# Optimization experiments

Hardware: AMD Instinct MI355X
Metric: run time of the kernel (lower is better)

Reference implementation:

```python
import jax, jax.numpy as jnp
import numpy as np

D_MODEL = 512
D_INNER = 1024           # expand=2 * d_model
HEADDIM = 1024           # headdim = 2*hidden_dim -> nheads = 1
NHEADS = 1
D_STATE = 128            # Mamba2 default
D_CONV = 4               # Mamba2 default
CONV_DIM = D_INNER + 2 * D_STATE   # 1280
D_IN_PROJ = 2 * D_INNER + 2 * D_STATE + NHEADS  # 2305
BATCH, SEQ = 8, 2048
EPS = 1e-5


def setup_inputs() -> dict:
    key = jax.random.key(0)
    ks = jax.random.split(key, 8)
    x = jax.random.normal(ks[0], (BATCH, SEQ, D_MODEL), dtype=jnp.float32)
    rnn_state = jnp.zeros((1, BATCH, D_MODEL), dtype=jnp.float32)
    W_in = jax.random.normal(ks[1], (D_MODEL, D_IN_PROJ), dtype=jnp.float32) * 0.02
    conv_w = jax.random.normal(ks[2], (CONV_DIM, D_CONV), dtype=jnp.float32) * 0.2
    conv_b = jnp.zeros((CONV_DIM,), dtype=jnp.float32)
    dt_bias = jax.random.normal(ks[3], (NHEADS,), dtype=jnp.float32) * 0.1
    # A in (-16, -1): A_log = log(uniform(1,16))
    A_log = jnp.log(jax.random.uniform(ks[4], (NHEADS,), minval=1.0, maxval=16.0, dtype=jnp.float32))
    D = jnp.ones((NHEADS,), dtype=jnp.float32)
    norm_w = jnp.ones((D_INNER,), dtype=jnp.float32)
    W_out = jax.random.normal(ks[5], (D_INNER, D_MODEL), dtype=jnp.float32) * 0.02
    return {"x": x, "rnn_state": rnn_state, "W_in": W_in, "conv_w": conv_w,
            "conv_b": conv_b, "dt_bias": dt_bias, "A_log": A_log, "D": D,
            "norm_w": norm_w, "W_out": W_out}


def _mamba2_forward(x, W_in, conv_w, conv_b, dt_bias, A_log, D, norm_w, W_out):
    Bsz, T, _ = x.shape
    zxbcdt = x @ W_in                              # [B,T,2305]
    z = zxbcdt[..., :D_INNER]                      # [B,T,1024]
    xBC = zxbcdt[..., D_INNER:D_INNER + CONV_DIM]  # [B,T,1280]
    dt = zxbcdt[..., -NHEADS:]                     # [B,T,1]

    # causal depthwise conv1d over time, then silu
    xBC_t = jnp.transpose(xBC, (0, 2, 1))          # [B,C,T]
    w = conv_w[:, None, :]                          # [C,1,K]
    conv = jax.lax.conv_general_dilated(
        xBC_t, w, window_strides=(1,), padding=[(D_CONV - 1, 0)],
        feature_group_count=CONV_DIM, dimension_numbers=("NCH", "OIH", "NCH"))
    xBC = jax.nn.silu(jnp.transpose(conv, (0, 2, 1)) + conv_b)  # [B,T,1280]

    x_ssm = xBC[..., :D_INNER].reshape(Bsz, T, NHEADS, HEADDIM)  # [B,T,H,P]
    Bm = xBC[..., D_INNER:D_INNER + D_STATE]       # [B,T,N] (ngroups=1)
    Cm = xBC[..., -D_STATE:]                       # [B,T,N]

    dt = jax.nn.softplus(dt + dt_bias)             # [B,T,H]
    A = -jnp.exp(A_log)                            # [H]

    # selective SSM recurrence over time (time-major scan)
    xs = (jnp.transpose(x_ssm, (1, 0, 2, 3)),      # [T,B,H,P]
          jnp.transpose(dt, (1, 0, 2)),            # [T,B,H]
          jnp.transpose(Bm, (1, 0, 2)),            # [T,B,N]
          jnp.transpose(Cm, (1, 0, 2)))            # [T,B,N]
    h0 = jnp.zeros((Bsz, NHEADS, HEADDIM, D_STATE), dtype=x.dtype)

    def step(h, inp):
        xt, dtt, Bt, Ct = inp
        dA = jnp.exp(dtt * A)                      # [B,H]
        h = h * dA[:, :, None, None] + (dtt[:, :, None] * xt)[..., None] * Bt[:, None, None, :]
        y = jnp.einsum("bhpn,bn->bhp", h, Ct)
        return h, y

    _, ys = jax.lax.scan(step, h0, xs)             # ys: [T,B,H,P]
    y = jnp.transpose(ys, (1, 0, 2, 3)) + x_ssm * D[None, None, :, None]
    y = y.reshape(Bsz, T, D_INNER)

    # gated RMSNorm (norm_before_gate=False): rmsnorm(y * silu(z)) * weight
    y = y * jax.nn.silu(z)
    y = y * jax.lax.rsqrt(jnp.mean(y * y, axis=-1, keepdims=True) + EPS) * norm_w
    return y @ W_out                               # [B,T,D_MODEL]


def reference(x, rnn_state, W_in, conv_w, conv_b, dt_bias, A_log, D, norm_w, W_out):
    out = _mamba2_forward(x, W_in, conv_w, conv_b, dt_bias, A_log, D, norm_w, W_out)
    return (out, rnn_state)
```

## Files before the change

kernel.cpp:

```cpp
#include <hip/hip_runtime.h>
#include <hip/hip_bf16.h>
#include <math.h>

#define D_MODEL 512
#define D_INNER 1024
#define D_STATE 128
#define CONV_DIM (D_INNER + 2*D_STATE)
#define D_IN_PROJ (2*D_INNER + 2*D_STATE + 1)
#define NPROJ 2304
#define BATCH 8
#define SEQ 2048
#define NROWS (BATCH*SEQ)
#define CHUNK 128
#define NCHUNK (NROWS/CHUNK)
#define CPB (SEQ/CHUNK)
#define EPS_RMS 1e-5f

typedef __hip_bfloat16 bf16;
typedef __attribute__((ext_vector_type(8))) short short8;
typedef __attribute__((ext_vector_type(4))) float f32x4;

__device__ __forceinline__ float fbf(bf16 v) { return __bfloat162float(v); }
__device__ __forceinline__ bf16 tbf(float v) { return __float2bfloat16(v); }

__device__ __forceinline__ void gl2lds16(const bf16* g, bf16* l) {
    __builtin_amdgcn_global_load_lds(
        (const __attribute__((address_space(1))) unsigned int*)g,
        (__attribute__((address_space(3))) unsigned int*)l, 16, 0, 0);
}

__global__ void k_transpose_cvt(const float* __restrict__ src, bf16* __restrict__ dst,
                                int R, int C, int sstride, const float* __restrict__ scale) {
    __shared__ float tile[32][33];
    int c0 = blockIdx.x * 32, r0 = blockIdx.y * 32;
    int tx = threadIdx.x, ty = threadIdx.y;
    #pragma unroll
    for (int i = 0; i < 32; i += 8) {
        float s = scale ? scale[c0 + ty + i] : 1.f;
        tile[ty + i][tx] = src[(size_t)(c0 + ty + i) * sstride + (r0 + tx)] * s;
    }
    __syncthreads();
    #pragma unroll
    for (int i = 0; i < 32; i += 8)
        dst[(size_t)(r0 + ty + i) * C + (c0 + tx)] = tbf(tile[tx][ty + i]);
}

__global__ __launch_bounds__(256) void k_dtcvt(
    const float* __restrict__ x, const float* __restrict__ W_in,
    const float* __restrict__ dt_bias,
    bf16* __restrict__ xb, float* __restrict__ dts)
{
    __shared__ float wcol[D_MODEL];
    int tid = threadIdx.x;
    wcol[tid]       = W_in[(size_t)tid * D_IN_PROJ + 2304];
    wcol[tid + 256] = W_in[(size_t)(tid + 256) * D_IN_PROJ + 2304];
    __syncthreads();
    int row  = blockIdx.x * 4 + (tid >> 6);
    int lane = tid & 63;
    const float* xr = x + (size_t)row * D_MODEL;
    float4 a = *(const float4*)(xr + lane * 8);
    float4 b = *(const float4*)(xr + lane * 8 + 4);
    union { bf16 o[8]; uint4 u; } pk;
    pk.o[0]=tbf(a.x); pk.o[1]=tbf(a.y); pk.o[2]=tbf(a.z); pk.o[3]=tbf(a.w);
    pk.o[4]=tbf(b.x); pk.o[5]=tbf(b.y); pk.o[6]=tbf(b.z); pk.o[7]=tbf(b.w);
    *(uint4*)(xb + (size_t)row * D_MODEL + lane * 8) = pk.u;
    const float* wc = wcol + lane * 8;
    float s = a.x*wc[0]+a.y*wc[1]+a.z*wc[2]+a.w*wc[3]
            + b.x*wc[4]+b.y*wc[5]+b.z*wc[6]+b.w*wc[7];
    #pragma unroll
    for (int off = 32; off; off >>= 1) s += __shfl_xor(s, off);
    if (lane == 0) {
        float raw = s + dt_bias[0];
        dts[row] = raw > 20.f ? raw : log1pf(expf(raw));
    }
}

template<int MODE>
__global__ __launch_bounds__(256) void k_bgemm(
    const bf16* __restrict__ A, int lda, size_t sA,
    const bf16* __restrict__ Bt, int ldb, size_t sB,
    void* __restrict__ Cv, int ldc, size_t sC, int K,
    const bf16* __restrict__ zg, float* __restrict__ ssq)
{
    constexpr int BK = 64;
    __shared__ __align__(16) bf16 As[128][BK];
    __shared__ __align__(16) bf16 Bs[128][BK];
    const int tid = threadIdx.x, lane = tid & 63, wave = tid >> 6;
    const int wm = (wave & 1) * 64, wn = (wave >> 1) * 64;
    const int lr = lane & 15, quad = lane >> 4;
    const int rx = lr & 7;
    const size_t bm = (size_t)blockIdx.x * 128;
    const size_t bn = (size_t)blockIdx.y * 128;
    const size_t bi = blockIdx.z;
    A  += bi * sA;
    Bt += bi * sB;
    const int srow = lane >> 3;
    const int scol = (((lane & 7) ^ srow) << 3);

    f32x4 acc[4][4];
    #pragma unroll
    for (int i = 0; i < 4; ++i)
        #pragma unroll
        for (int j = 0; j < 4; ++j) acc[i][j] = (f32x4){0.f,0.f,0.f,0.f};

    for (int k0 = 0; k0 < K; k0 += BK) {
        __syncthreads();
        #pragma unroll
        for (int q = 0; q < 4; ++q) {
            int rg = wave * 32 + q * 8;
            gl2lds16(A  + (bm + rg + srow) * lda + k0 + scol, &As[rg][0]);
            gl2lds16(Bt + (bn + rg + srow) * ldb + k0 + scol, &Bs[rg][0]);
        }
        __syncthreads();
        #pragma unroll
        for (int ks = 0; ks < BK; ks += 32) {
            const int off = ((((ks >> 3) + quad) ^ rx) << 3);
            short8 af[4], bg[4];
            #pragma unroll
            for (int i = 0; i < 4; ++i)
                af[i] = *(const short8*)(&As[wm + i*16 + lr][off]);
            #pragma unroll
            for (int j = 0; j < 4; ++j)
                bg[j] = *(const short8*)(&Bs[wn + j*16 + lr][off]);
            #pragma unroll
            for (int i = 0; i < 4; ++i)
                #pragma unroll
                for (int j = 0; j < 4; ++j)
                    acc[i][j] = __builtin_amdgcn_mfma_f32_16x16x32_bf16(af[i], bg[j], acc[i][j], 0,0,0);
        }
    }
    if (MODE <= 1) {
        #pragma unroll
        for (int i = 0; i < 4; ++i)
            #pragma unroll
            for (int j = 0; j < 4; ++j)
                #pragma unroll
                for (int r = 0; r < 4; ++r) {
                    size_t row = bm + wm + i*16 + quad*4 + r;
                    size_t col = bn + wn + j*16 + lr;
                    float v = acc[i][j][r];
                    if (MODE == 0) ((float*)Cv + bi*sC)[row * ldc + col] = v;
                    else           ((bf16*)Cv + bi*sC)[row * ldc + col] = tbf(v);
                }
    } else if (MODE == 2) {
        const size_t tokbase = bi * CHUNK;
        float srw[4][4];
        #pragma unroll
        for (int i = 0; i < 4; ++i)
            #pragma unroll
            for (int r = 0; r < 4; ++r) srw[i][r] = 0.f;
        #pragma unroll
        for (int i = 0; i < 4; ++i)
            #pragma unroll
            for (int j = 0; j < 4; ++j)
                #pragma unroll
                for (int r = 0; r < 4; ++r) {
                    size_t row = bm + wm + i*16 + quad*4 + r;
                    size_t col = bn + wn + j*16 + lr;
                    float z = fbf(zg[(tokbase + row) * D_INNER + col]);
                    float g = acc[i][j][r] * z / (1.f + expf(-z));
                    ((bf16*)Cv + bi*sC)[row * ldc + col] = tbf(g);
                    srw[i][r] += g * g;
                }
        #pragma unroll
        for (int i = 0; i < 4; ++i)
            #pragma unroll
            for (int r = 0; r < 4; ++r) {
                float s = srw[i][r];
                s += __shfl_xor(s, 1);
                s += __shfl_xor(s, 2);
                s += __shfl_xor(s, 4);
                s += __shfl_xor(s, 8);
                if (lr == 0)
                    atomicAdd(ssq + tokbase + bm + wm + i*16 + quad*4 + r, s);
            }
    } else {
        #pragma unroll
        for (int i = 0; i < 4; ++i)
            #pragma unroll
            for (int r = 0; r < 4; ++r) {
                size_t row = bm + wm + i*16 + quad*4 + r;
                float sc = rsqrtf(ssq[row] * (1.f / D_INNER) + EPS_RMS);
                #pragma unroll
                for (int j = 0; j < 4; ++j) {
                    size_t col = bn + wn + j*16 + lr;
                    ((float*)Cv + bi*sC)[row * ldc + col] = acc[i][j][r] * sc;
                }
            }
    }
}

__global__ __launch_bounds__(256) void k_gemm_in(
    const bf16* __restrict__ A, const bf16* __restrict__ Bt,
    bf16* __restrict__ zb, bf16* __restrict__ xBCin, int K)
{
    constexpr int BK = 64;
    __shared__ __align__(16) bf16 As[128][BK];
    __shared__ __align__(16) bf16 Bs[128][BK];
    const int tid = threadIdx.x, lane = tid & 63, wave = tid >> 6;
    const int wm = (wave & 1) * 64, wn = (wave >> 1) * 64;
    const int lr = lane & 15, quad = lane >> 4;
    const int rx = lr & 7;
    const size_t bm = (size_t)blockIdx.x * 128;
    const int bn = blockIdx.y * 128;
    const int srow = lane >> 3;
    const int scol = (((lane & 7) ^ srow) << 3);

    f32x4 acc[4][4];
    #pragma unroll
    for (int i = 0; i < 4; ++i)
        #pragma unroll
        for (int j = 0; j < 4; ++j) acc[i][j] = (f32x4){0.f,0.f,0.f,0.f};

    for (int k0 = 0; k0 < K; k0 += BK) {
        __syncthreads();
        #pragma unroll
        for (int q = 0; q < 4; ++q) {
            int rg = wave * 32 + q * 8;
            gl2lds16(A  + (bm + rg + srow) * K + k0 + scol, &As[rg][0]);
            gl2lds16(Bt + ((size_t)bn + rg + srow) * K + k0 + scol, &Bs[rg][0]);
        }
        __syncthreads();
        #pragma unroll
        for (int ks = 0; ks < BK; ks += 32) {
            const int off = ((((ks >> 3) + quad) ^ rx) << 3);
            short8 af[4], bg[4];
            #pragma unroll
            for (int i = 0; i < 4; ++i)
                af[i] = *(const short8*)(&As[wm + i*16 + lr][off]);
            #pragma unroll
            for (int j = 0; j < 4; ++j)
                bg[j] = *(const short8*)(&Bs[wn + j*16 + lr][off]);
            #pragma unroll
            for (int i = 0; i < 4; ++i)
                #pragma unroll
                for (int j = 0; j < 4; ++j)
                    acc[i][j] = __builtin_amdgcn_mfma_f32_16x16x32_bf16(af[i], bg[j], acc[i][j], 0,0,0);
        }
    }
    #pragma unroll
    for (int i = 0; i < 4; ++i)
        #pragma unroll
        for (int j = 0; j < 4; ++j)
            #pragma unroll
            for (int r = 0; r < 4; ++r) {
                size_t row = bm + wm + i*16 + quad*4 + r;
                int col = bn + wn + j*16 + lr;
                float v = acc[i][j][r];
                if (col < D_INNER) zb[row * D_INNER + col] = tbf(v);
                else xBCin[row * CONV_DIM + (col - D_INNER)] = tbf(v);
            }
}

__global__ void k_prep(const float* __restrict__ dts, const float* __restrict__ A_log,
                       float* __restrict__ svec, float* __restrict__ wvec,
                       float* __restrict__ esvec, float* __restrict__ Pc)
{
    int chunk = blockIdx.x, t = threadIdx.x;
    int row = chunk * CHUNK + t;
    float A = -expf(A_log[0]);
    __shared__ float sh[CHUNK];
    sh[t] = A * dts[row];
    __syncthreads();
    for (int off = 1; off < CHUNK; off <<= 1) {
        float v = (t >= off) ? sh[t - off] : 0.f;
        __syncthreads();
        sh[t] += v;
        __syncthreads();
    }
    float s = sh[t], sL = sh[CHUNK - 1];
    svec[row]  = s;
    wvec[row]  = expf(sL - s) * dts[row];
    esvec[row] = expf(s);
    if (t == CHUNK - 1) Pc[chunk] = expf(sL);
}

__global__ __launch_bounds__(256) void k_ssd_bc(
    const bf16* __restrict__ xBCin, const float* __restrict__ conv_w,
    const float* __restrict__ conv_b, const float* __restrict__ wvec,
    const float* __restrict__ esvec, const float* __restrict__ svec,
    const float* __restrict__ dts, const float* __restrict__ Dp,
    bf16* __restrict__ Bw, bf16* __restrict__ A2)
{
    __shared__ __align__(16) bf16 Ls[131][128];
    __shared__ __align__(16) bf16 Bts[128][136];
    __shared__ __align__(16) bf16 Cts[128][136];
    __shared__ float sv_s[128], dt_s[128], wv_s[128], es_s[128];
    const int chunk = blockIdx.x;
    const int tid = threadIdx.x;
    const bool first = (chunk % CPB) == 0;
    const size_t rowbase = (size_t)chunk * CHUNK;
    if (tid < 128) {
        sv_s[tid] = svec[rowbase + tid];
        dt_s[tid] = dts[rowbase + tid];
        wv_s[tid] = wvec[rowbase + tid];
        es_s[tid] = esvec[rowbase + tid];
    }
    const int ch  = tid & 127;
    const int seg = tid >> 7;

    #pragma unroll
    for (int phase = 0; phase < 2; ++phase) {
        const int coff = D_INNER + phase * 128;
        __syncthreads();
        for (int i = tid; i < 131 * 16; i += 256) {
            int r = i >> 4, cg = (i & 15) << 3;
            uint4 v = (uint4){0,0,0,0};
            if (!(first && r < 3))
                v = *(const uint4*)(xBCin + (rowbase + r - 3) * CONV_DIM + coff + cg);
            *(uint4*)(&Ls[r][cg]) = v;
        }
        __syncthreads();
        float4 w = *(const float4*)(conv_w + (coff + ch) * 4);
        float bias = conv_b[coff + ch];
        float xv[11];
        #pragma unroll
        for (int i = 0; i < 3; ++i) xv[i + 8] = fbf(Ls[seg * 64 + i][ch]);
        for (int v = 0; v < 8; ++v) {
            int t0 = seg * 64 + v * 8;
            xv[0]=xv[8]; xv[1]=xv[9]; xv[2]=xv[10];
            #pragma unroll
            for (int i = 3; i < 11; ++i) xv[i] = fbf(Ls[t0 + i][ch]);
            float o[8];
            #pragma unroll
            for (int j = 0; j < 8; ++j) {
                float a = bias + w.x*xv[j] + w.y*xv[j+1] + w.z*xv[j+2] + w.w*xv[j+3];
                o[j] = a / (1.f + expf(-a));
            }
            if (phase == 0) {
                union { bf16 ob[8]; uint4 u; } pk;
                #pragma unroll
                for (int j = 0; j < 8; ++j) {
                    Bts[t0 + j][ch] = tbf(o[j]);
                    pk.ob[j] = tbf(o[j] * wv_s[t0 + j]);
                }
                *(uint4*)(Bw + (size_t)chunk*(D_STATE*CHUNK) + (size_t)ch*CHUNK + t0) = pk.u;
            } else {
                #pragma unroll
                for (int j = 0; j < 8; ++j) {
                    Cts[t0 + j][ch] = tbf(o[j]);
                    A2[(size_t)chunk*(CHUNK*256) + (size_t)(t0+j)*256 + 128 + ch] =
                        tbf(o[j] * es_s[t0 + j]);
                }
            }
        }
    }
    __syncthreads();
    const int lane = tid & 63, wave = tid >> 6;
    const int wm = (wave & 1) * 64, wn = (wave >> 1) * 64;
    const int lr = lane & 15, quad = lane >> 4;
    f32x4 acc[4][4];
    #pragma unroll
    for (int i = 0; i < 4; ++i)
        #pragma unroll
        for (int j = 0; j < 4; ++j) acc[i][j] = (f32x4){0.f,0.f,0.f,0.f};
    #pragma unroll
    for (int ks = 0; ks < 128; ks += 32) {
        short8 af[4], bg[4];
        #pragma unroll
        for (int i = 0; i < 4; ++i)
            af[i] = *(const short8*)(&Cts[wm + i*16 + lr][ks + quad*8]);
        #pragma unroll
        for (int j = 0; j < 4; ++j)
            bg[j] = *(const short8*)(&Bts[wn + j*16 + lr][ks + quad*8]);
        #pragma unroll
        for (int i = 0; i < 4; ++i)
            #pragma unroll
            for (int j = 0; j < 4; ++j)
                acc[i][j] = __builtin_amdgcn_mfma_f32_16x16x32_bf16(af[i], bg[j], acc[i][j], 0,0,0);
    }
    const float D0 = Dp[0];
    #pragma unroll
    for (int i = 0; i < 4; ++i)
        #pragma unroll
        for (int j = 0; j < 4; ++j)
            #pragma unroll
            for (int r = 0; r < 4; ++r) {
                int t = wm + i*16 + quad*4 + r;
                int u = wn + j*16 + lr;
                float o = 0.f;
                if (u <= t) {
                    o = acc[i][j][r] * expf(sv_s[t] - sv_s[u]) * dt_s[u];
                    if (u == t) o += D0;
                }
                A2[(size_t)chunk*(CHUNK*256) + (size_t)t*256 + u] = tbf(o);
            }
}

__global__ __launch_bounds__(256) void k_conv_xdh(
    const bf16* __restrict__ xBCin, const float* __restrict__ conv_w,
    const float* __restrict__ conv_b, const bf16* __restrict__ Bw,
    bf16* __restrict__ B2, bf16* __restrict__ dH)
{
    __shared__ __align__(16) bf16 Ls[131][128];
    __shared__ __align__(16) bf16 Xs[128][136];
    const int chunk = blockIdx.y;
    const int p0 = blockIdx.x * 128;
    const int tid = threadIdx.x;
    const bool first = (chunk % CPB) == 0;
    const size_t rowbase = (size_t)chunk * CHUNK;
    for (int i = tid; i < 131 * 16; i += 256) {
        int r = i >> 4, cg = (i & 15) << 3;
        uint4 v = (uint4){0,0,0,0};
        if (!(first && r < 3))
            v = *(const uint4*)(xBCin + (rowbase + r - 3) * CONV_DIM + p0 + cg);
        *(uint4*)(&Ls[r][cg]) = v;
    }
    __syncthreads();
    const int p = tid & 127;
    const int half = tid >> 7;
    const int ch = p0 + p;
    float4 w = *(const float4*)(conv_w + ch * 4);
    float bias = conv_b[ch];
    bf16* outrow = B2 + (size_t)chunk * (D_INNER * 256) + (size_t)ch * 256;
    float xv[11];
    #pragma unroll
    for (int i = 0; i < 3; ++i) xv[i + 8] = fbf(Ls[half * 64 + i][p]);
    for (int v = 0; v < 8; ++v) {
        int t0 = half * 64 + v * 8;
        xv[0]=xv[8]; xv[1]=xv[9]; xv[2]=xv[10];
        #pragma unroll
        for (int i = 3; i < 11; ++i) xv[i] = fbf(Ls[t0 + i][p]);
        union { bf16 o[8]; uint4 u; } pk;
        #pragma unroll
        for (int j = 0; j < 8; ++j) {
            float a = bias + w.x*xv[j] + w.y*xv[j+1] + w.z*xv[j+2] + w.w*xv[j+3];
            pk.o[j] = tbf(a / (1.f + expf(-a)));
        }
        *(uint4*)(outrow + t0) = pk.u;
        *(uint4*)(&Xs[p][t0]) = pk.u;
    }
    __syncthreads();
    const int lane = tid & 63, wave = tid >> 6;
    const int wm = (wave & 1) * 64, wn = (wave >> 1) * 64;
    const int lr = lane & 15, quad = lane >> 4;
    const bf16* bwc = Bw + (size_t)chunk * (D_STATE * CHUNK);
    f32x4 acc[4][4];
    #pragma unroll
    for (int i = 0; i < 4; ++i)
        #pragma unroll
        for (int j = 0; j < 4; ++j) acc[i][j] = (f32x4){0.f,0.f,0.f,0.f};
    #pragma unroll
    for (int ks = 0; ks < 128; ks += 32) {
        short8 af[4], bg[4];
        #pragma unroll
        for (int j = 0; j < 4; ++j)
            bg[j] = *(const short8*)(bwc + (size_t)(wn + j*16 + lr) * CHUNK + ks + quad*8);
        #pragma unroll
        for (int i = 0; i < 4; ++i)
            af[i] = *(const short8*)(&Xs[wm + i*16 + lr][ks + quad*8]);
        #pragma unroll
        for (int i = 0; i < 4; ++i)
            #pragma unroll
            for (int j = 0; j < 4; ++j)
                acc[i][j] = __builtin_amdgcn_mfma_f32_16x16x32_bf16(af[i], bg[j], acc[i][j], 0,0,0);
    }
    #pragma unroll
    for (int i = 0; i < 4; ++i)
        #pragma unroll
        for (int j = 0; j < 4; ++j)
            #pragma unroll
            for (int r = 0; r < 4; ++r) {
                int pr = p0 + wm + i*16 + quad*4 + r;
                int n  = wn + j*16 + lr;
                dH[(size_t)chunk*(D_INNER*D_STATE) + (size_t)pr*D_STATE + n] = tbf(acc[i][j][r]);
            }
}

__global__ __launch_bounds__(256) void k_carry(
    const bf16* __restrict__ dH, const float* __restrict__ Pc, bf16* __restrict__ B2)
{
    int idx = blockIdx.x * 256 + threadIdx.x;
    int b = blockIdx.y;
    int p = idx >> 4, ng = (idx & 15) << 3;
    uint4 v[CPB];
    float pc[CPB];
    #pragma unroll
    for (int c = 0; c < CPB; ++c)
        v[c] = *(const uint4*)(dH + (size_t)(b*CPB + c)*(D_INNER*D_STATE) + (size_t)p*D_STATE + ng);
    #pragma unroll
    for (int c = 0; c < CPB; ++c) pc[c] = Pc[b*CPB + c];
    float h[8] = {0,0,0,0,0,0,0,0};
    #pragma unroll
    for (int c = 0; c < CPB; ++c) {
        union { bf16 o[8]; uint4 u; } pk;
        #pragma unroll
        for (int k = 0; k < 8; ++k) pk.o[k] = tbf(h[k]);
        *(uint4*)(B2 + (size_t)(b*CPB + c)*(D_INNER*256) + (size_t)p*256 + 128 + ng) = pk.u;
        const bf16* vb = (const bf16*)&v[c];
        #pragma unroll
        for (int k = 0; k < 8; ++k) h[k] = pc[c]*h[k] + fbf(vb[k]);
    }
}

extern "C" void kernel_launch(void* const* d_in, const int* in_sizes, int n_in,
                              void* d_out, int out_size, void* d_ws, size_t ws_size,
                              hipStream_t stream)
{
    const float* x       = (const float*)d_in[0];
    const float* rnn     = (const float*)d_in[1];
    const float* W_in    = (const float*)d_in[2];
    const float* conv_w  = (const float*)d_in[3];
    const float* conv_b  = (const float*)d_in[4];
    const float* dt_bias = (const float*)d_in[5];
    const float* A_log   = (const float*)d_in[6];
    const float* Dp      = (const float*)d_in[7];
    const float* norm_w  = (const float*)d_in[8];
    const float* W_out   = (const float*)d_in[9];
    float* out = (float*)d_out;

    char* ws = (char*)d_ws;
    size_t off = 0;
    auto alloc = [&](size_t bytes) { void* p = ws + off; off += (bytes + 255) & ~255ULL; return p; };

    bf16*  W_inbT  = (bf16*) alloc((size_t)NPROJ * D_MODEL * 2);
    bf16*  W_outbT = (bf16*) alloc((size_t)D_MODEL * D_INNER * 2);
    float* dts     = (float*)alloc((size_t)NROWS * 4);
    float* svec    = (float*)alloc((size_t)NROWS * 4);
    float* wvec    = (float*)alloc((size_t)NROWS * 4);
    float* esvec   = (float*)alloc((size_t)NROWS * 4);
    float* Pc      = (float*)alloc((size_t)NCHUNK * 4);
    float* ssq     = (float*)alloc((size_t)NROWS * 4);
    bf16*  zb      = (bf16*) alloc((size_t)NROWS * D_INNER * 2);
    bf16*  A2      = (bf16*) alloc((size_t)NCHUNK * CHUNK * 256 * 2);
    bf16*  B2      = (bf16*) alloc((size_t)NCHUNK * D_INNER * 256 * 2);
    bf16*  Bw      = (bf16*) alloc((size_t)NCHUNK * D_STATE * CHUNK * 2);
    char* RA = (char*)alloc((size_t)NROWS * D_MODEL * 2 + (size_t)NROWS * D_INNER * 2);
    bf16*  xb   = (bf16*)RA;
    bf16*  dH   = (bf16*)(RA + (size_t)NROWS * D_MODEL * 2);
    bf16*  ybf  = (bf16*)RA;
    bf16*  xBCin = (bf16*)alloc((size_t)NROWS * CONV_DIM * 2);

    hipMemsetAsync(ssq, 0, (size_t)NROWS * sizeof(float), stream);

    k_dtcvt<<<NROWS / 4, 256, 0, stream>>>(x, W_in, dt_bias, xb, dts);
    k_transpose_cvt<<<dim3(D_MODEL/32, NPROJ/32), dim3(32, 8), 0, stream>>>(
        W_in, W_inbT, NPROJ, D_MODEL, D_IN_PROJ, nullptr);
    k_transpose_cvt<<<dim3(D_INNER/32, D_MODEL/32), dim3(32, 8), 0, stream>>>(
        W_out, W_outbT, D_MODEL, D_INNER, D_MODEL, norm_w);
    k_prep<<<NCHUNK, CHUNK, 0, stream>>>(dts, A_log, svec, wvec, esvec, Pc);

    k_gemm_in<<<dim3(NROWS/128, NPROJ/128), 256, 0, stream>>>(xb, W_inbT, zb, xBCin, D_MODEL);

    k_ssd_bc<<<NCHUNK, 256, 0, stream>>>(xBCin, conv_w, conv_b, wvec, esvec,
                                         svec, dts, Dp, Bw, A2);

    k_conv_xdh<<<dim3(8, NCHUNK), 256, 0, stream>>>(xBCin, conv_w, conv_b, Bw, B2, dH);

    k_carry<<<dim3(64, BATCH), 256, 0, stream>>>(dH, Pc, B2);

    k_bgemm<2><<<dim3(1, D_INNER/128, NCHUNK), 256, 0, stream>>>(
        A2, 256, (size_t)CHUNK*256,
        B2, 256, (size_t)D_INNER*256,
        ybf, D_INNER, (size_t)CHUNK*D_INNER, 256, zb, ssq);

    k_bgemm<3><<<dim3(NROWS/128, D_MODEL/128, 1), 256, 0, stream>>>(
        ybf, D_INNER, 0, W_outbT, D_INNER, 0, out, D_MODEL, 0, D_INNER,
        nullptr, ssq);

    hipMemcpyAsync(out + (size_t)NROWS * D_MODEL, rnn,
                   (size_t)BATCH * D_MODEL * sizeof(float),
                   hipMemcpyDeviceToDevice, stream);
}
```

Measured before the change: 321.1 us.

## Merge prologue launches, stage gate z via LDS, use fast exp/rcp intrinsics

Merges the two weight transpose-convert launches and the rnn_state copy into one prologue kernel. The ssq memset moves into k_dtcvt, and the gated epilogue of the batched GEMM now loads z through swizzled LDS with global_load_lds instead of scattered global reads. expf and divisions are replaced by __expf and hardware reciprocal, and the X tile in k_conv_xdh gets an XOR swizzle instead of padding. The aim is fewer launches, less uncoalesced z traffic and cheaper transcendentals, at the cost of slightly lower exp/rcp precision.

```diff
diff --git a/kernel.cpp b/kernel.cpp
--- a/kernel.cpp
+++ b/kernel.cpp
@@ -22,6 +22,9 @@
 
 __device__ __forceinline__ float fbf(bf16 v) { return __bfloat162float(v); }
 __device__ __forceinline__ bf16 tbf(float v) { return __float2bfloat16(v); }
+__device__ __forceinline__ float fexp(float x) { return __expf(x); }
+__device__ __forceinline__ float frcp(float x) { return __builtin_amdgcn_rcpf(x); }
+__device__ __forceinline__ float fsilu(float a) { return a * frcp(1.f + fexp(-a)); }
 
 __device__ __forceinline__ void gl2lds16(const bf16* g, bf16* l) {
     __builtin_amdgcn_global_load_lds(
@@ -29,11 +32,32 @@
         (__attribute__((address_space(3))) unsigned int*)l, 16, 0, 0);
 }
 
-__global__ void k_transpose_cvt(const float* __restrict__ src, bf16* __restrict__ dst,
-                                int R, int C, int sstride, const float* __restrict__ scale) {
+__global__ __launch_bounds__(256) void k_prologue(
+    const float* __restrict__ W_in, const float* __restrict__ W_out,
+    const float* __restrict__ norm_w, const float* __restrict__ rnn,
+    bf16* __restrict__ W_inbT, bf16* __restrict__ W_outbT, float* __restrict__ outTail)
+{
+    int b = blockIdx.x;
+    if (b == 1152 + 512) {
+        int tid = threadIdx.x;
+        #pragma unroll
+        for (int i = 0; i < 4; ++i)
+            *(float4*)(outTail + (tid + i * 256) * 4) =
+                *(const float4*)(rnn + (tid + i * 256) * 4);
+        return;
+    }
     __shared__ float tile[32][33];
-    int c0 = blockIdx.x * 32, r0 = blockIdx.y * 32;
-    int tx = threadIdx.x, ty = threadIdx.y;
+    const float* src; bf16* dst; const float* scale;
+    int c0, r0, sstride, C;
+    if (b < 1152) {
+        src = W_in; dst = W_inbT; scale = nullptr;
+        c0 = (b % 16) * 32; r0 = (b / 16) * 32; sstride = D_IN_PROJ; C = D_MODEL;
+    } else {
+        int bb = b - 1152;
+        src = W_out; dst = W_outbT; scale = norm_w;
+        c0 = (bb % 32) * 32; r0 = (bb / 32) * 32; sstride = D_MODEL; C = D_INNER;
+    }
+    int tx = threadIdx.x & 31, ty = threadIdx.x >> 5;
     #pragma unroll
     for (int i = 0; i < 32; i += 8) {
         float s = scale ? scale[c0 + ty + i] : 1.f;
@@ -48,7 +72,7 @@
 __global__ __launch_bounds__(256) void k_dtcvt(
     const float* __restrict__ x, const float* __restrict__ W_in,
     const float* __restrict__ dt_bias,
-    bf16* __restrict__ xb, float* __restrict__ dts)
+    bf16* __restrict__ xb, float* __restrict__ dts, float* __restrict__ ssq)
 {
     __shared__ float wcol[D_MODEL];
     int tid = threadIdx.x;
@@ -71,7 +95,8 @@
     for (int off = 32; off; off >>= 1) s += __shfl_xor(s, off);
     if (lane == 0) {
         float raw = s + dt_bias[0];
-        dts[row] = raw > 20.f ? raw : log1pf(expf(raw));
+        dts[row] = raw > 20.f ? raw : log1pf(fexp(raw));
+        ssq[row] = 0.f;
     }
 }
 
@@ -83,8 +108,9 @@
     const bf16* __restrict__ zg, float* __restrict__ ssq)
 {
     constexpr int BK = 64;
-    __shared__ __align__(16) bf16 As[128][BK];
-    __shared__ __align__(16) bf16 Bs[128][BK];
+    __shared__ __align__(16) bf16 SM[128 * 128];
+    bf16* As = SM;
+    bf16* Bs = SM + 8192;
     const int tid = threadIdx.x, lane = tid & 63, wave = tid >> 6;
     const int wm = (wave & 1) * 64, wn = (wave >> 1) * 64;
     const int lr = lane & 15, quad = lane >> 4;
@@ -108,8 +134,8 @@
         #pragma unroll
         for (int q = 0; q < 4; ++q) {
             int rg = wave * 32 + q * 8;
-            gl2lds16(A  + (bm + rg + srow) * lda + k0 + scol, &As[rg][0]);
-            gl2lds16(Bt + (bn + rg + srow) * ldb + k0 + scol, &Bs[rg][0]);
+            gl2lds16(A  + (bm + rg + srow) * lda + k0 + scol, As + rg * BK);
+            gl2lds16(Bt + (bn + rg + srow) * ldb + k0 + scol, Bs + rg * BK);
         }
         __syncthreads();
         #pragma unroll
@@ -118,10 +144,10 @@
             short8 af[4], bg[4];
             #pragma unroll
             for (int i = 0; i < 4; ++i)
-                af[i] = *(const short8*)(&As[wm + i*16 + lr][off]);
+                af[i] = *(const short8*)(As + (wm + i*16 + lr) * BK + off);
             #pragma unroll
             for (int j = 0; j < 4; ++j)
-                bg[j] = *(const short8*)(&Bs[wn + j*16 + lr][off]);
+                bg[j] = *(const short8*)(Bs + (wn + j*16 + lr) * BK + off);
             #pragma unroll
             for (int i = 0; i < 4; ++i)
                 #pragma unroll
@@ -144,6 +170,16 @@
                 }
     } else if (MODE == 2) {
         const size_t tokbase = bi * CHUNK;
+        const bf16* zrow = zg + tokbase * D_INNER + bn;
+        __syncthreads();
+        #pragma unroll
+        for (int q = 0; q < 8; ++q) {
+            int r0 = wave * 32 + q * 4;
+            int rr = r0 + (lane >> 4);
+            int gl = (lane & 15) ^ (rr & 7);
+            gl2lds16(zrow + (size_t)rr * D_INNER + gl * 8, SM + r0 * 128);
+        }
+        __syncthreads();
         float srw[4][4];
         #pragma unroll
         for (int i = 0; i < 4; ++i)
@@ -155,11 +191,12 @@
             for (int j = 0; j < 4; ++j)
                 #pragma unroll
                 for (int r = 0; r < 4; ++r) {
-                    size_t row = bm + wm + i*16 + quad*4 + r;
-                    size_t col = bn + wn + j*16 + lr;
-                    float z = fbf(zg[(tokbase + row) * D_INNER + col]);
-                    float g = acc[i][j][r] * z / (1.f + expf(-z));
-                    ((bf16*)Cv + bi*sC)[row * ldc + col] = tbf(g);
+                    int row = wm + i*16 + quad*4 + r;
+                    int col = wn + j*16 + lr;
+                    int gph = ((col >> 3) ^ (row & 7));
+                    float z = fbf(SM[row * 128 + (gph << 3) + (col & 7)]);
+                    float g = acc[i][j][r] * z * frcp(1.f + fexp(-z));
+                    ((bf16*)Cv + bi*sC)[(size_t)row * ldc + bn + col] = tbf(g);
                     srw[i][r] += g * g;
                 }
         #pragma unroll
@@ -172,7 +209,7 @@
                 s += __shfl_xor(s, 4);
                 s += __shfl_xor(s, 8);
                 if (lr == 0)
-                    atomicAdd(ssq + tokbase + bm + wm + i*16 + quad*4 + r, s);
+                    atomicAdd(ssq + tokbase + wm + i*16 + quad*4 + r, s);
             }
     } else {
         #pragma unroll
@@ -258,7 +295,7 @@
 {
     int chunk = blockIdx.x, t = threadIdx.x;
     int row = chunk * CHUNK + t;
-    float A = -expf(A_log[0]);
+    float A = -fexp(A_log[0]);
     __shared__ float sh[CHUNK];
     sh[t] = A * dts[row];
     __syncthreads();
@@ -270,9 +307,9 @@
     }
     float s = sh[t], sL = sh[CHUNK - 1];
     svec[row]  = s;
-    wvec[row]  = expf(sL - s) * dts[row];
-    esvec[row] = expf(s);
-    if (t == CHUNK - 1) Pc[chunk] = expf(sL);
+    wvec[row]  = fexp(sL - s) * dts[row];
+    esvec[row] = fexp(s);
+    if (t == CHUNK - 1) Pc[chunk] = fexp(sL);
 }
 
 __global__ __launch_bounds__(256) void k_ssd_bc(
@@ -325,7 +362,7 @@
             #pragma unroll
             for (int j = 0; j < 8; ++j) {
                 float a = bias + w.x*xv[j] + w.y*xv[j+1] + w.z*xv[j+2] + w.w*xv[j+3];
-                o[j] = a / (1.f + expf(-a));
+                o[j] = fsilu(a);
             }
             if (phase == 0) {
                 union { bf16 ob[8]; uint4 u; } pk;
@@ -380,7 +417,7 @@
                 int u = wn + j*16 + lr;
                 float o = 0.f;
                 if (u <= t) {
-                    o = acc[i][j][r] * expf(sv_s[t] - sv_s[u]) * dt_s[u];
+                    o = acc[i][j][r] * fexp(sv_s[t] - sv_s[u]) * dt_s[u];
                     if (u == t) o += D0;
                 }
                 A2[(size_t)chunk*(CHUNK*256) + (size_t)t*256 + u] = tbf(o);
@@ -393,7 +430,7 @@
     bf16* __restrict__ B2, bf16* __restrict__ dH)
 {
     __shared__ __align__(16) bf16 Ls[131][128];
-    __shared__ __align__(16) bf16 Xs[128][136];
+    __shared__ __align__(16) bf16 XsF[128 * 128];
     const int chunk = blockIdx.y;
     const int p0 = blockIdx.x * 128;
     const int tid = threadIdx.x;
@@ -425,10 +462,10 @@
         #pragma unroll
         for (int j = 0; j < 8; ++j) {
             float a = bias + w.x*xv[j] + w.y*xv[j+1] + w.z*xv[j+2] + w.w*xv[j+3];
-            pk.o[j] = tbf(a / (1.f + expf(-a)));
+            pk.o[j] = tbf(fsilu(a));
         }
         *(uint4*)(outrow + t0) = pk.u;
-        *(uint4*)(&Xs[p][t0]) = pk.u;
+        *(uint4*)(&XsF[p * 128 + ((((t0 >> 3) ^ (p & 7))) << 3)]) = pk.u;
     }
     __syncthreads();
     const int lane = tid & 63, wave = tid >> 6;
@@ -448,7 +485,8 @@
             bg[j] = *(const short8*)(bwc + (size_t)(wn + j*16 + lr) * CHUNK + ks + quad*8);
         #pragma unroll
         for (int i = 0; i < 4; ++i)
-            af[i] = *(const short8*)(&Xs[wm + i*16 + lr][ks + quad*8]);
+            af[i] = *(const short8*)(&XsF[(wm + i*16 + lr) * 128 +
+                                          (((((ks >> 3) + quad) ^ (lr & 7))) << 3)]);
         #pragma unroll
         for (int i = 0; i < 4; ++i)
             #pragma unroll
@@ -531,13 +569,9 @@
     bf16*  ybf  = (bf16*)RA;
     bf16*  xBCin = (bf16*)alloc((size_t)NROWS * CONV_DIM * 2);
 
-    hipMemsetAsync(ssq, 0, (size_t)NROWS * sizeof(float), stream);
-
-    k_dtcvt<<<NROWS / 4, 256, 0, stream>>>(x, W_in, dt_bias, xb, dts);
-    k_transpose_cvt<<<dim3(D_MODEL/32, NPROJ/32), dim3(32, 8), 0, stream>>>(
-        W_in, W_inbT, NPROJ, D_MODEL, D_IN_PROJ, nullptr);
-    k_transpose_cvt<<<dim3(D_INNER/32, D_MODEL/32), dim3(32, 8), 0, stream>>>(
-        W_out, W_outbT, D_MODEL, D_INNER, D_MODEL, norm_w);
+    k_dtcvt<<<NROWS / 4, 256, 0, stream>>>(x, W_in, dt_bias, xb, dts, ssq);
+    k_prologue<<<1152 + 512 + 1, 256, 0, stream>>>(
+        W_in, W_out, norm_w, rnn, W_inbT, W_outbT, out + (size_t)NROWS * D_MODEL);
     k_prep<<<NCHUNK, CHUNK, 0, stream>>>(dts, A_log, svec, wvec, esvec, Pc);
 
     k_gemm_in<<<dim3(NROWS/128, NPROJ/128), 256, 0, stream>>>(xb, W_inbT, zb, xBCin, D_MODEL);
@@ -557,8 +591,4 @@
     k_bgemm<3><<<dim3(NROWS/128, D_MODEL/128, 1), 256, 0, stream>>>(
         ybf, D_INNER, 0, W_outbT, D_INNER, 0, out, D_MODEL, 0, D_INNER,
         nullptr, ssq);
-
-    hipMemcpyAsync(out + (size_t)NROWS * D_MODEL, rnn,
-                   (size_t)BATCH * D_MODEL * sizeof(float),
-                   hipMemcpyDeviceToDevice, stream);
-}
+}
```

Result: faster. 300.2 us (-6.5%).
